# Kernel optimization log

Hardware: AMD Instinct MI355X
Metric: run time of the kernel (lower is better)

## Reference

```python
import jax, jax.numpy as jnp
from jax import lax
import numpy as np

B, T, D, S, P = 2048, 64, 512, 256, 11
H1 = (D + S) // 2  # position head hidden = (d_model + state_dim)//2 = 384


def setup_inputs() -> dict:
    key = jax.random.key(0)
    ks = jax.random.split(key, 8)
    return {
        "price_features": jax.random.normal(ks[0], (B, T, D), jnp.float32),
        "u": jax.random.uniform(ks[1], (B, T, P), jnp.float32),  # gumbel uniform noise
        "W1": 0.02 * jax.random.normal(ks[2], (H1, D + S), jnp.float32),
        "b1": jnp.zeros((H1,), jnp.float32),
        "W2": 0.02 * jax.random.normal(ks[3], (P, H1), jnp.float32),
        "b2": jnp.zeros((P,), jnp.float32),
        "temperature": jnp.float32(1.0),
        "W_ih": 0.05 * jax.random.normal(ks[4], (3 * S, D + 1), jnp.float32),
        "b_ih": jnp.zeros((3 * S,), jnp.float32),
        "W_hh": 0.05 * jax.random.normal(ks[5], (3 * S, S), jnp.float32),
        "b_hh": jnp.zeros((3 * S,), jnp.float32),
        "h0": jax.random.normal(ks[6], (S,), jnp.float32),  # strategy_state_init
    }


def reference(price_features, u, W1, b1, W2, b2, temperature, W_ih, b_ih, W_hh, b_hh, h0):
    pos_vals = jnp.arange(P, dtype=jnp.float32)
    batch = price_features.shape[0]
    h_init = jnp.broadcast_to(h0, (batch, S))

    def step(h, xs):
        feat, u_t = xs  # feat: [B,D], u_t: [B,P]
        combined = jnp.concatenate([feat, h], axis=-1)          # [B, D+S]
        hidden = jax.nn.relu(combined @ W1.T + b1)              # [B, H1]
        logits = hidden @ W2.T + b2                             # [B, P]
        gumbel = -jnp.log(-jnp.log(u_t + 1e-20) + 1e-20)
        probs = jax.nn.softmax((logits + gumbel) / temperature, axis=-1)
        pos = probs @ pos_vals                                  # [B] expected position
        x = jnp.concatenate([feat, pos[:, None]], axis=-1)      # [B, D+1]
        gi = x @ W_ih.T + b_ih                                  # [B, 3S]
        gh = h @ W_hh.T + b_hh                                  # [B, 3S]
        i_r, i_z, i_n = jnp.split(gi, 3, axis=-1)
        h_r, h_z, h_n = jnp.split(gh, 3, axis=-1)
        r = jax.nn.sigmoid(i_r + h_r)
        z = jax.nn.sigmoid(i_z + h_z)
        n = jnp.tanh(i_n + r * h_n)
        h_new = (1.0 - z) * n + z * h                           # PyTorch GRUCell update
        return h_new, (pos, h_new)

    feats_t = jnp.swapaxes(price_features, 0, 1)  # [T,B,D]
    u_tfirst = jnp.swapaxes(u, 0, 1)              # [T,B,P]
    h_final, (positions, states) = lax.scan(step, h_init, (feats_t, u_tfirst))
    all_expected_positions = jnp.swapaxes(positions, 0, 1)  # [B,T]
    all_strategy_states = jnp.swapaxes(states, 0, 1)        # [B,T,S]
    return all_expected_positions, all_strategy_states, h_final
```

## Files before the change

### kernel.cpp

```cpp
#include <hip/hip_runtime.h>
#include <stdint.h>

#define B_  2048
#define T_  64
#define D_  512
#define S_  256
#define P_  11
#define H1_ 384
#define NG_ 1152
#define KH_ 256

typedef unsigned short ushort_t;
typedef __attribute__((ext_vector_type(4))) float    f32x4;
typedef __attribute__((ext_vector_type(8))) __bf16   bf16x8;
typedef __attribute__((ext_vector_type(8))) unsigned short u16x8;

static __device__ __forceinline__ ushort_t f2bf(float f) {
    uint32_t u = __builtin_bit_cast(uint32_t, f);
    u += 0x7fffu + ((u >> 16) & 1u);
    return (ushort_t)(u >> 16);
}
static __device__ __forceinline__ float bf2f(ushort_t h) {
    uint32_t u = ((uint32_t)h) << 16;
    return __builtin_bit_cast(float, u);
}
static __device__ __forceinline__ u16x8 ntload8(const ushort_t* p) {
    return __builtin_nontemporal_load((const u16x8*)p);
}
static __device__ __forceinline__ void gload16(const ushort_t* g, ushort_t* l) {
    __builtin_amdgcn_global_load_lds(
        (const __attribute__((address_space(1))) uint32_t*)(const void*)g,
        (__attribute__((address_space(3))) uint32_t*)(void*)l,
        16, 0, 0);
}


__global__ __launch_bounds__(256) void convert_feat(
        const float* __restrict__ feat,
        ushort_t* __restrict__ featS) {
    int base = blockIdx.x * 1024 + threadIdx.x;
    #pragma unroll
    for (int k = 0; k < 4; ++k) {
        int o = base + k * 256;
        int tile = o >> 10;
        int s = o & 1023;
        int row = s >> 3, slot = s & 7;
        int mtile = tile >> 3, kt = tile & 7;
        int col = kt * 64 + (((slot ^ (row & 7))) << 3);
        const float* gp = feat + (size_t)(mtile * 128 + row) * 512 + col;
        f32x4 f0 = *(const f32x4*)gp;
        f32x4 f1 = *(const f32x4*)(gp + 4);
        u16x8 ov;
        #pragma unroll
        for (int j = 0; j < 4; ++j) { ov[j] = f2bf(f0[j]); ov[4 + j] = f2bf(f1[j]); }
        __builtin_nontemporal_store(ov, (u16x8*)(featS + (size_t)o * 8));
    }
}

__global__ void pack_weights(const float* __restrict__ W1,
                             const float* __restrict__ Wih,
                             const float* __restrict__ Whh,
                             ushort_t* __restrict__ WcatS,
                             ushort_t* __restrict__ WhBp) {
    int idx = blockIdx.x * 256 + threadIdx.x;
    const int tot1 = NG_ * D_;
    if (idx < tot1) {
        int tile = idx >> 13;
        int e = idx & 8191;
        int row = e >> 6, slot = (e >> 3) & 7, j = e & 7;
        int ntile = tile >> 3, kt = tile & 7;
        int col = kt * 64 + ((slot ^ (row & 7)) << 3) + j;
        int n = ntile * 128 + row;
        float v = (n < H1_) ? W1[n * 768 + col] : Wih[(n - H1_) * 513 + col];
        WcatS[idx] = f2bf(v);
    } else {
        int i = idx - tot1;
        int j  = i & 7;
        int l  = (i >> 3) & 63;
        int kc = (i >> 9) & 7;
        int nt = i >> 12;
        int row = nt * 16 + (l & 15);
        int col = kc * 32 + (l >> 4) * 8 + j;
        float v = (row < H1_) ? W1[row * 768 + 512 + col] : Whh[(row - H1_) * 256 + col];
        WhBp[i] = f2bf(v);
    }
}

__global__ __launch_bounds__(256) void gemm_pre(
        const ushort_t* __restrict__ featS,
        const ushort_t* __restrict__ WcatS,
        ushort_t* __restrict__ pre) {
    __shared__ __attribute__((aligned(16))) ushort_t As[8192];
    __shared__ __attribute__((aligned(16))) ushort_t Bs[8192];

    int bx = blockIdx.x;
    int xcd = bx & 7, slt = bx >> 3;
    int mt = (slt / 9) * 8 + xcd;
    int ntb = slt % 9;
    int m0 = mt * 128, n0 = ntb * 128;

    int tid = threadIdx.x;
    int lane = tid & 63, wave = tid >> 6;
    int wr = wave >> 1, wc = wave & 1;
    int l15 = lane & 15, q = lane >> 4;

    const ushort_t* Abase = featS + (size_t)mt * 8 * 8192 + (size_t)(lane << 3);
    const ushort_t* Bbase = WcatS + (size_t)ntb * 8 * 8192 + (size_t)(lane << 3);

    f32x4 acc[4][4];
    #pragma unroll
    for (int i = 0; i < 4; ++i)
        #pragma unroll
        for (int j = 0; j < 4; ++j)
            acc[i][j] = (f32x4){0.f, 0.f, 0.f, 0.f};

    const int swz = (l15 & 7) << 4;

    for (int kt = 0; kt < 8; ++kt) {
        #pragma unroll
        for (int i = 0; i < 4; ++i) {
            int c = wave * 4 + i;
            gload16(Abase + (size_t)kt * 8192 + (c << 9), &As[c << 9]);
            gload16(Bbase + (size_t)kt * 8192 + (c << 9), &Bs[c << 9]);
        }
        __syncthreads();
        #pragma unroll
        for (int kc = 0; kc < 2; ++kc) {
            const int coff = (kc * 64 + q * 16) ^ swz;
            bf16x8 af[4], bfr[4];
            #pragma unroll
            for (int i = 0; i < 4; ++i)
                af[i] = __builtin_bit_cast(bf16x8, *(const u16x8*)(
                    (const char*)As + (wr * 64 + i * 16 + l15) * 128 + coff));
            #pragma unroll
            for (int j = 0; j < 4; ++j)
                bfr[j] = __builtin_bit_cast(bf16x8, *(const u16x8*)(
                    (const char*)Bs + (wc * 64 + j * 16 + l15) * 128 + coff));
            #pragma unroll
            for (int i = 0; i < 4; ++i)
                #pragma unroll
                for (int j = 0; j < 4; ++j)
                    acc[i][j] = __builtin_amdgcn_mfma_f32_16x16x32_bf16(
                        af[i], bfr[j], acc[i][j], 0, 0, 0);
        }
        __syncthreads();
    }
    #pragma unroll
    for (int i = 0; i < 4; ++i) {
        #pragma unroll
        for (int r = 0; r < 4; ++r) {
            int m = m0 + wr * 64 + i * 16 + q * 4 + r;
            int orow = (m & 63) * 2048 + (m >> 6);
            ushort_t* op = pre + (size_t)orow * NG_ + n0 + wc * 64 + l15;
            #pragma unroll
            for (int j = 0; j < 4; ++j)
                __builtin_nontemporal_store(f2bf(acc[i][j][r]), &op[j * 16]);
        }
    }
}

__global__ __launch_bounds__(1024, 4) void recurrent(
        const float* __restrict__ u,
        const float* __restrict__ b1,
        const float* __restrict__ W2,
        const float* __restrict__ b2,
        const float* __restrict__ temp_p,
        const float* __restrict__ Wih,
        const float* __restrict__ bih,
        const float* __restrict__ bhh,
        const float* __restrict__ h0,
        const ushort_t* __restrict__ WhBp,
        const ushort_t* __restrict__ pre,
        float* __restrict__ out_pos,
        float* __restrict__ out_states,
        float* __restrict__ out_hfin) {
    __shared__ __attribute__((aligned(16))) ushort_t gates[8][1160];
    __shared__ __attribute__((aligned(16))) ushort_t preg[8][1160];
    __shared__ __attribute__((aligned(16))) float    hf[8][256];
    __shared__ __attribute__((aligned(16))) ushort_t hb[16][264];
    __shared__ __attribute__((aligned(16))) ushort_t hidb[16][392];
    __shared__ __attribute__((aligned(16))) ushort_t w2s[16][392];
    __shared__ __attribute__((aligned(16))) float    b1s[384];
    __shared__ __attribute__((aligned(16))) float    wps[768];
    __shared__ __attribute__((aligned(16))) float    bihs[768];
    __shared__ __attribute__((aligned(16))) float    bhhs[768];
    __shared__ float    b2s[16];
    __shared__ float    logit_s[8][17];
    __shared__ float    pos_s[8];
    __shared__ float    u_s[8][12];

    const int tid  = threadIdx.x;
    const int lane = tid & 63, wave = tid >> 6;
    const int l15  = lane & 15, q = lane >> 4;
    const int row8 = tid >> 7;
    const int ln128 = tid & 127;
    const int b0 = blockIdx.x * 8;

    for (int i = tid; i < 384; i += 1024) b1s[i] = b1[i];
    for (int i = tid; i < 768; i += 1024) {
        wps[i]  = Wih[i * 513 + 512];
        bihs[i] = bih[i];
        bhhs[i] = bhh[i];
    }
    if (tid < 11) b2s[tid] = b2[tid];
    for (int i = tid; i < 16 * 392; i += 1024) {
        int r = i / 392, c = i - r * 392;
        float v = (r < 11 && c < 384) ? W2[r * 384 + c] : 0.f;
        w2s[r][c] = f2bf(v);
    }
    for (int i = tid; i < 8 * 256; i += 1024) {
        int m = i >> 8, s = i & 255;
        float v = h0[s];
        hf[m][s] = v;
        hb[m][s] = f2bf(v);
    }
    for (int i = tid; i < 8 * 264; i += 1024) {
        int m = 8 + i / 264;
        hb[m][i % 264] = 0;
    }
    for (int i = tid; i < 8 * 392; i += 1024) {
        int m = 8 + i / 392;
        hidb[m][i % 392] = 0;
    }
    float tinv = 1.0f / temp_p[0];

    u16x8 pr[2];
    {
        const size_t prow = (size_t)b0;
        #pragma unroll
        for (int r = 0; r < 2; ++r) {
            int c = tid + (r << 10);
            if (c < 1152) {
                int row = c / 144, off = c - row * 144;
                pr[r] = ntload8(pre + (prow + row) * NG_ + (size_t)off * 8);
            }
        }
    }
    float uval = 0.f;
    const int um = tid / 11, up = tid - um * 11;
    if (tid < 88) uval = u[((size_t)(b0 + um) * 64 + 0) * 11 + up];
    __syncthreads();

    for (int t = 0; t < 64; ++t) {
        #pragma unroll
        for (int r = 0; r < 2; ++r) {
            int c = tid + (r << 10);
            if (c < 1152) {
                int row = c / 144, off = c - row * 144;
                *(u16x8*)&preg[row][off * 8] = pr[r];
            }
        }
        if (tid < 88) u_s[um][up] = uval;

        bf16x8 af[8];
        #pragma unroll
        for (int kc = 0; kc < 8; ++kc)
            af[kc] = __builtin_bit_cast(bf16x8, *(const u16x8*)&hb[l15][kc * 32 + q * 8]);

        for (int nt = wave; nt < 24; nt += 16) {
            f32x4 acc = (f32x4){0.f, 0.f, 0.f, 0.f};
            const ushort_t* wp = WhBp + (((size_t)nt * 8) << 9) + (lane << 3);
            #pragma unroll
            for (int kc = 0; kc < 8; ++kc) {
                bf16x8 bfr = __builtin_bit_cast(bf16x8, *(const u16x8*)(wp + ((size_t)kc << 9)));
                acc = __builtin_amdgcn_mfma_f32_16x16x32_bf16(af[kc], bfr, acc, 0, 0, 0);
            }
            if (q < 2) {
                int n = nt * 16 + l15;
                #pragma unroll
                for (int r = 0; r < 4; ++r)
                    gates[q * 4 + r][n] = f2bf(acc[r]);
            }
        }
        __syncthreads();

        if (ln128 < 48) {
            int c = ln128 << 3;
            u16x8 g8 = *(const u16x8*)&gates[row8][c];
            u16x8 p8 = *(const u16x8*)&preg[row8][c];
            f32x4 ba = *(const f32x4*)&b1s[c];
            f32x4 bb = *(const f32x4*)&b1s[c + 4];
            u16x8 o;
            #pragma unroll
            for (int jj = 0; jj < 8; ++jj) {
                float bv = (jj < 4) ? ba[jj] : bb[jj - 4];
                float v = bf2f(g8[jj]) + bf2f(p8[jj]) + bv;
                o[jj] = f2bf(fmaxf(v, 0.f));
            }
            *(u16x8*)&hidb[row8][c] = o;
        }
        __syncthreads();

        if (wave == 0) {
            f32x4 lacc = (f32x4){0.f, 0.f, 0.f, 0.f};
            #pragma unroll
            for (int kc = 0; kc < 12; ++kc) {
                bf16x8 ha = __builtin_bit_cast(bf16x8,
                    *(const u16x8*)&hidb[l15][kc * 32 + q * 8]);
                bf16x8 wb = __builtin_bit_cast(bf16x8,
                    *(const u16x8*)&w2s[l15][kc * 32 + q * 8]);
                lacc = __builtin_amdgcn_mfma_f32_16x16x32_bf16(ha, wb, lacc, 0, 0, 0);
            }
            if (q < 2) {
                #pragma unroll
                for (int r = 0; r < 4; ++r)
                    logit_s[q * 4 + r][l15] = lacc[r];
            }
            __builtin_amdgcn_s_waitcnt(0);
            if (lane < 8) {
                int m = lane;
                float lg[11];
                float mx = -1e30f;
                #pragma unroll
                for (int p = 0; p < 11; ++p) {
                    float uu = u_s[m][p];
                    float g = -__logf(-__logf(uu + 1e-20f) + 1e-20f);
                    float a = (logit_s[m][p] + b2s[p] + g) * tinv;
                    lg[p] = a;
                    mx = fmaxf(mx, a);
                }
                float se = 0.f, sp = 0.f;
                #pragma unroll
                for (int p = 0; p < 11; ++p) {
                    float e = __expf(lg[p] - mx);
                    se += e;
                    sp += e * (float)p;
                }
                float pos = sp / se;
                pos_s[m] = pos;
                __builtin_nontemporal_store(pos, &out_pos[(size_t)(b0 + m) * 64 + t]);
            }
        } else {
            for (int nt = 23 + wave; nt < 72; nt += 15) {
                f32x4 acc = (f32x4){0.f, 0.f, 0.f, 0.f};
                const ushort_t* wp = WhBp + (((size_t)nt * 8) << 9) + (lane << 3);
                #pragma unroll
                for (int kc = 0; kc < 8; ++kc) {
                    bf16x8 bfr = __builtin_bit_cast(bf16x8, *(const u16x8*)(wp + ((size_t)kc << 9)));
                    acc = __builtin_amdgcn_mfma_f32_16x16x32_bf16(af[kc], bfr, acc, 0, 0, 0);
                }
                if (q < 2) {
                    int n = nt * 16 + l15;
                    #pragma unroll
                    for (int r = 0; r < 4; ++r)
                        gates[q * 4 + r][n] = f2bf(acc[r]);
                }
            }
        }

        if (t < 63) {
            const size_t prow = (size_t)(t + 1) * 2048 + b0;
            #pragma unroll
            for (int r = 0; r < 2; ++r) {
                int c = tid + (r << 10);
                if (c < 1152) {
                    int row = c / 144, off = c - row * 144;
                    pr[r] = ntload8(pre + (prow + row) * NG_ + (size_t)off * 8);
                }
            }
            if (tid < 88) uval = u[((size_t)(b0 + um) * 64 + (t + 1)) * 11 + up];
        }
        __syncthreads();

        {
            float pos = pos_s[row8];
            float* st = out_states + ((size_t)(b0 + row8) * 64 + t) * 256;
            #pragma unroll
            for (int j = 0; j < 2; ++j) {
                int s = ln128 + (j << 7);
                float ar  = bf2f(preg[row8][384 + s]) + bihs[s]
                          + bf2f(gates[row8][384 + s]) + bhhs[s];
                float az  = bf2f(preg[row8][640 + s]) + bihs[256 + s]
                          + bf2f(gates[row8][640 + s]) + bhhs[256 + s];
                float in0 = bf2f(preg[row8][896 + s]) + bihs[512 + s];
                float gn  = bf2f(gates[row8][896 + s]) + bhhs[512 + s];
                float hp  = hf[row8][s];
                float rr = __builtin_amdgcn_rcpf(1.f + __expf(-(ar + pos * wps[s])));
                float zz = __builtin_amdgcn_rcpf(1.f + __expf(-(az + pos * wps[256 + s])));
                float xn = in0 + pos * wps[512 + s] + rr * gn;
                float e2 = __expf(2.f * xn);
                float nn = 1.f - 2.f * __builtin_amdgcn_rcpf(e2 + 1.f);
                float hnew = (1.f - zz) * nn + zz * hp;
                hf[row8][s] = hnew;
                hb[row8][s] = f2bf(hnew);
                __builtin_nontemporal_store(hnew, st + s);
            }
        }
        __syncthreads();
    }

    for (int i = tid; i < 8 * 256; i += 1024) {
        int m = i >> 8, s = i & 255;
        __builtin_nontemporal_store(hf[m][s], &out_hfin[(size_t)(b0 + m) * 256 + s]);
    }
}

extern "C" void kernel_launch(void* const* d_in, const int* in_sizes, int n_in,
                              void* d_out, int out_size, void* d_ws, size_t ws_size,
                              hipStream_t stream) {
    const float* feat = (const float*)d_in[0];
    const float* u    = (const float*)d_in[1];
    const float* W1   = (const float*)d_in[2];
    const float* b1   = (const float*)d_in[3];
    const float* W2   = (const float*)d_in[4];
    const float* b2   = (const float*)d_in[5];
    const float* temp = (const float*)d_in[6];
    const float* Wih  = (const float*)d_in[7];
    const float* bih  = (const float*)d_in[8];
    const float* Whh  = (const float*)d_in[9];
    const float* bhh  = (const float*)d_in[10];
    const float* h0   = (const float*)d_in[11];

    ushort_t* WcatS = (ushort_t*)d_ws;
    ushort_t* WhBp  = WcatS + NG_ * D_;
    ushort_t* pre   = WhBp + NG_ * KH_;
    ushort_t* featS = pre + (size_t)T_ * B_ * NG_;

    float* out_pos    = (float*)d_out;
    float* out_states = out_pos + (size_t)B_ * T_;
    float* out_hfin   = out_states + (size_t)B_ * T_ * S_;

    pack_weights<<<3456, 256, 0, stream>>>(W1, Wih, Whh, WcatS, WhBp);
    convert_feat<<<8192, 256, 0, stream>>>(feat, featS);
    gemm_pre<<<9216, 256, 0, stream>>>(featS, WcatS, pre);
    recurrent<<<256, 1024, 0, stream>>>(u, b1, W2, b2, temp, Wih, bih, bhh, h0,
                                        WhBp, pre, out_pos, out_states, out_hfin);
}
```

Before: 1.107 ms.

## Pre-pack GEMM operands in MFMA fragment order and double-buffer recurrent prefetch

Feature and weight tensors are now packed directly in per-lane MFMA fragment order, so gemm_pre reads its operands straight from global memory into registers and no longer stages them through LDS with barriers. The pre-activation output is written in batch-major order, so each recurrent block reads contiguous rows across timesteps. In the recurrent kernel, the hidden-layer ReLU is fused into the W1 MFMA tile epilogue, which removes a separate gate pass. The next step's pre-activations and noise are double-buffered in shared memory, which eliminates a copy at the top of each step. The cost is that gemm_pre gives up LDS reuse and relies on cache hits, loading each operand fragment separately per wave.

```diff
diff --git a/kernel.cpp b/kernel.cpp
--- a/kernel.cpp
+++ b/kernel.cpp
@@ -27,52 +27,55 @@
 static __device__ __forceinline__ u16x8 ntload8(const ushort_t* p) {
     return __builtin_nontemporal_load((const u16x8*)p);
 }
-static __device__ __forceinline__ void gload16(const ushort_t* g, ushort_t* l) {
-    __builtin_amdgcn_global_load_lds(
-        (const __attribute__((address_space(1))) uint32_t*)(const void*)g,
-        (__attribute__((address_space(3))) uint32_t*)(void*)l,
-        16, 0, 0);
-}
 
 
 __global__ __launch_bounds__(256) void convert_feat(
         const float* __restrict__ feat,
-        ushort_t* __restrict__ featS) {
+        ushort_t* __restrict__ featP) {
     int base = blockIdx.x * 1024 + threadIdx.x;
     #pragma unroll
     for (int k = 0; k < 4; ++k) {
         int o = base + k * 256;
-        int tile = o >> 10;
-        int s = o & 1023;
-        int row = s >> 3, slot = s & 7;
-        int mtile = tile >> 3, kt = tile & 7;
-        int col = kt * 64 + (((slot ^ (row & 7))) << 3);
-        const float* gp = feat + (size_t)(mtile * 128 + row) * 512 + col;
-        f32x4 f0 = *(const f32x4*)gp;
-        f32x4 f1 = *(const f32x4*)(gp + 4);
+        int mt = o >> 13;
+        int f = o & 8191;
+        int ln = f & 63;
+        int i = (f >> 6) & 3;
+        int half = (f >> 8) & 1;
+        int kc = (f >> 9) & 1;
+        int kt = f >> 10;
+        int row = half * 64 + i * 16 + (ln & 15);
+        int col = kt * 64 + kc * 32 + ((ln >> 4) << 3);
+        const float* gp = feat + (size_t)(mt * 128 + row) * 512 + col;
+        f32x4 f0 = __builtin_nontemporal_load((const f32x4*)gp);
+        f32x4 f1 = __builtin_nontemporal_load((const f32x4*)(gp + 4));
         u16x8 ov;
         #pragma unroll
         for (int j = 0; j < 4; ++j) { ov[j] = f2bf(f0[j]); ov[4 + j] = f2bf(f1[j]); }
-        __builtin_nontemporal_store(ov, (u16x8*)(featS + (size_t)o * 8));
+        __builtin_nontemporal_store(ov, (u16x8*)(featP + (size_t)o * 8));
     }
 }
 
 __global__ void pack_weights(const float* __restrict__ W1,
                              const float* __restrict__ Wih,
                              const float* __restrict__ Whh,
-                             ushort_t* __restrict__ WcatS,
+                             ushort_t* __restrict__ WcatP,
                              ushort_t* __restrict__ WhBp) {
     int idx = blockIdx.x * 256 + threadIdx.x;
     const int tot1 = NG_ * D_;
     if (idx < tot1) {
-        int tile = idx >> 13;
-        int e = idx & 8191;
-        int row = e >> 6, slot = (e >> 3) & 7, j = e & 7;
-        int ntile = tile >> 3, kt = tile & 7;
-        int col = kt * 64 + ((slot ^ (row & 7)) << 3) + j;
+        int o = idx >> 3, j = idx & 7;
+        int ntile = o >> 13;
+        int f = o & 8191;
+        int ln = f & 63;
+        int i = (f >> 6) & 3;
+        int half = (f >> 8) & 1;
+        int kc = (f >> 9) & 1;
+        int kt = f >> 10;
+        int row = half * 64 + i * 16 + (ln & 15);
+        int col = kt * 64 + kc * 32 + ((ln >> 4) << 3) + j;
         int n = ntile * 128 + row;
         float v = (n < H1_) ? W1[n * 768 + col] : Wih[(n - H1_) * 513 + col];
-        WcatS[idx] = f2bf(v);
+        WcatP[idx] = f2bf(v);
     } else {
         int i = idx - tot1;
         int j  = i & 7;
@@ -86,13 +89,10 @@
     }
 }
 
-__global__ __launch_bounds__(256) void gemm_pre(
-        const ushort_t* __restrict__ featS,
-        const ushort_t* __restrict__ WcatS,
+__global__ __launch_bounds__(256, 3) void gemm_pre(
+        const ushort_t* __restrict__ featP,
+        const ushort_t* __restrict__ WcatP,
         ushort_t* __restrict__ pre) {
-    __shared__ __attribute__((aligned(16))) ushort_t As[8192];
-    __shared__ __attribute__((aligned(16))) ushort_t Bs[8192];
-
     int bx = blockIdx.x;
     int xcd = bx & 7, slt = bx >> 3;
     int mt = (slt / 9) * 8 + xcd;
@@ -104,8 +104,8 @@
     int wr = wave >> 1, wc = wave & 1;
     int l15 = lane & 15, q = lane >> 4;
 
-    const ushort_t* Abase = featS + (size_t)mt * 8 * 8192 + (size_t)(lane << 3);
-    const ushort_t* Bbase = WcatS + (size_t)ntb * 8 * 8192 + (size_t)(lane << 3);
+    const ushort_t* Ab = featP + ((size_t)mt << 16) + (size_t)(lane << 3);
+    const ushort_t* Bb = WcatP + ((size_t)ntb << 16) + (size_t)(lane << 3);
 
     f32x4 acc[4][4];
     #pragma unroll
@@ -114,28 +114,19 @@
         for (int j = 0; j < 4; ++j)
             acc[i][j] = (f32x4){0.f, 0.f, 0.f, 0.f};
 
-    const int swz = (l15 & 7) << 4;
-
+    #pragma unroll
     for (int kt = 0; kt < 8; ++kt) {
         #pragma unroll
-        for (int i = 0; i < 4; ++i) {
-            int c = wave * 4 + i;
-            gload16(Abase + (size_t)kt * 8192 + (c << 9), &As[c << 9]);
-            gload16(Bbase + (size_t)kt * 8192 + (c << 9), &Bs[c << 9]);
-        }
-        __syncthreads();
-        #pragma unroll
         for (int kc = 0; kc < 2; ++kc) {
-            const int coff = (kc * 64 + q * 16) ^ swz;
             bf16x8 af[4], bfr[4];
             #pragma unroll
             for (int i = 0; i < 4; ++i)
                 af[i] = __builtin_bit_cast(bf16x8, *(const u16x8*)(
-                    (const char*)As + (wr * 64 + i * 16 + l15) * 128 + coff));
+                    Ab + ((((kt * 2 + kc) * 2 + wr) * 4 + i) << 9)));
             #pragma unroll
             for (int j = 0; j < 4; ++j)
                 bfr[j] = __builtin_bit_cast(bf16x8, *(const u16x8*)(
-                    (const char*)Bs + (wc * 64 + j * 16 + l15) * 128 + coff));
+                    Bb + ((((kt * 2 + kc) * 2 + wc) * 4 + j) << 9)));
             #pragma unroll
             for (int i = 0; i < 4; ++i)
                 #pragma unroll
@@ -143,15 +134,13 @@
                     acc[i][j] = __builtin_amdgcn_mfma_f32_16x16x32_bf16(
                         af[i], bfr[j], acc[i][j], 0, 0, 0);
         }
-        __syncthreads();
     }
     #pragma unroll
     for (int i = 0; i < 4; ++i) {
         #pragma unroll
         for (int r = 0; r < 4; ++r) {
             int m = m0 + wr * 64 + i * 16 + q * 4 + r;
-            int orow = (m & 63) * 2048 + (m >> 6);
-            ushort_t* op = pre + (size_t)orow * NG_ + n0 + wc * 64 + l15;
+            ushort_t* op = pre + (size_t)m * NG_ + n0 + wc * 64 + l15;
             #pragma unroll
             for (int j = 0; j < 4; ++j)
                 __builtin_nontemporal_store(f2bf(acc[i][j][r]), &op[j * 16]);
@@ -174,8 +163,8 @@
         float* __restrict__ out_pos,
         float* __restrict__ out_states,
         float* __restrict__ out_hfin) {
-    __shared__ __attribute__((aligned(16))) ushort_t gates[8][1160];
-    __shared__ __attribute__((aligned(16))) ushort_t preg[8][1160];
+    __shared__ __attribute__((aligned(16))) ushort_t gates[8][776];
+    __shared__ __attribute__((aligned(16))) ushort_t preg[2][8][1160];
     __shared__ __attribute__((aligned(16))) float    hf[8][256];
     __shared__ __attribute__((aligned(16))) ushort_t hb[16][264];
     __shared__ __attribute__((aligned(16))) ushort_t hidb[16][392];
@@ -187,7 +176,7 @@
     __shared__ float    b2s[16];
     __shared__ float    logit_s[8][17];
     __shared__ float    pos_s[8];
-    __shared__ float    u_s[8][12];
+    __shared__ float    u_s[2][8][12];
 
     const int tid  = threadIdx.x;
     const int lane = tid & 63, wave = tid >> 6;
@@ -224,70 +213,76 @@
     }
     float tinv = 1.0f / temp_p[0];
 
+    const int um = tid / 11, up = tid - um * 11;
     u16x8 pr[2];
     {
-        const size_t prow = (size_t)b0;
         #pragma unroll
         for (int r = 0; r < 2; ++r) {
             int c = tid + (r << 10);
             if (c < 1152) {
                 int row = c / 144, off = c - row * 144;
-                pr[r] = ntload8(pre + (prow + row) * NG_ + (size_t)off * 8);
-            }
-        }
-    }
-    float uval = 0.f;
-    const int um = tid / 11, up = tid - um * 11;
-    if (tid < 88) uval = u[((size_t)(b0 + um) * 64 + 0) * 11 + up];
-    __syncthreads();
-
-    for (int t = 0; t < 64; ++t) {
+                pr[r] = ntload8(pre + ((size_t)(b0 + row) * 64 + 0) * NG_ + (size_t)off * 8);
+            }
+        }
         #pragma unroll
         for (int r = 0; r < 2; ++r) {
             int c = tid + (r << 10);
             if (c < 1152) {
                 int row = c / 144, off = c - row * 144;
-                *(u16x8*)&preg[row][off * 8] = pr[r];
-            }
-        }
-        if (tid < 88) u_s[um][up] = uval;
+                *(u16x8*)&preg[0][row][off * 8] = pr[r];
+            }
+        }
+        if (tid < 88) u_s[0][um][up] = u[((size_t)(b0 + um) * 64 + 0) * 11 + up];
+    }
+    __syncthreads();
+
+    for (int t = 0; t < 64; ++t) {
+        const int cur = t & 1, nxt = cur ^ 1;
 
         bf16x8 af[8];
         #pragma unroll
         for (int kc = 0; kc < 8; ++kc)
             af[kc] = __builtin_bit_cast(bf16x8, *(const u16x8*)&hb[l15][kc * 32 + q * 8]);
 
-        for (int nt = wave; nt < 24; nt += 16) {
+        auto mfma_tile = [&](int nt) -> f32x4 {
+            const ushort_t* wp = WhBp + ((size_t)nt << 12) + (lane << 3);
             f32x4 acc = (f32x4){0.f, 0.f, 0.f, 0.f};
-            const ushort_t* wp = WhBp + (((size_t)nt * 8) << 9) + (lane << 3);
             #pragma unroll
             for (int kc = 0; kc < 8; ++kc) {
-                bf16x8 bfr = __builtin_bit_cast(bf16x8, *(const u16x8*)(wp + ((size_t)kc << 9)));
+                bf16x8 bfr = __builtin_bit_cast(bf16x8, *(const u16x8*)(wp + (kc << 9)));
                 acc = __builtin_amdgcn_mfma_f32_16x16x32_bf16(af[kc], bfr, acc, 0, 0, 0);
             }
+            return acc;
+        };
+        auto do_relu = [&](int nt) {
+            f32x4 acc = mfma_tile(nt);
             if (q < 2) {
                 int n = nt * 16 + l15;
                 #pragma unroll
+                for (int r = 0; r < 4; ++r) {
+                    int row = q * 4 + r;
+                    float v = acc[r] + bf2f(preg[cur][row][n]) + b1s[n];
+                    hidb[row][n] = f2bf(fmaxf(v, 0.f));
+                }
+            }
+        };
+        auto do_gates = [&](int nt) {
+            f32x4 acc = mfma_tile(nt);
+            if (q < 2) {
+                int n = (nt - 24) * 16 + l15;
+                #pragma unroll
                 for (int r = 0; r < 4; ++r)
                     gates[q * 4 + r][n] = f2bf(acc[r]);
             }
-        }
-        __syncthreads();
-
-        if (ln128 < 48) {
-            int c = ln128 << 3;
-            u16x8 g8 = *(const u16x8*)&gates[row8][c];
-            u16x8 p8 = *(const u16x8*)&preg[row8][c];
-            f32x4 ba = *(const f32x4*)&b1s[c];
-            f32x4 bb = *(const f32x4*)&b1s[c + 4];
-            u16x8 o;
-            #pragma unroll
-            for (int jj = 0; jj < 8; ++jj) {
-                float bv = (jj < 4) ? ba[jj] : bb[jj - 4];
-                float v = bf2f(g8[jj]) + bf2f(p8[jj]) + bv;
-                o[jj] = f2bf(fmaxf(v, 0.f));
-            }
-            *(u16x8*)&hidb[row8][c] = o;
+        };
+
+        if (wave == 0) {
+            do_relu(0); do_relu(1); do_relu(2);
+        } else {
+            int nt = 3 + (wave - 1);
+            do_relu(nt);
+            nt += 15;
+            if (nt < 24) do_relu(nt);
         }
         __syncthreads();
 
@@ -313,7 +308,7 @@
                 float mx = -1e30f;
                 #pragma unroll
                 for (int p = 0; p < 11; ++p) {
-                    float uu = u_s[m][p];
+                    float uu = u_s[cur][m][p];
                     float g = -__logf(-__logf(uu + 1e-20f) + 1e-20f);
                     float a = (logit_s[m][p] + b2s[p] + g) * tinv;
                     lg[p] = a;
@@ -331,31 +326,20 @@
                 __builtin_nontemporal_store(pos, &out_pos[(size_t)(b0 + m) * 64 + t]);
             }
         } else {
-            for (int nt = 23 + wave; nt < 72; nt += 15) {
-                f32x4 acc = (f32x4){0.f, 0.f, 0.f, 0.f};
-                const ushort_t* wp = WhBp + (((size_t)nt * 8) << 9) + (lane << 3);
-                #pragma unroll
-                for (int kc = 0; kc < 8; ++kc) {
-                    bf16x8 bfr = __builtin_bit_cast(bf16x8, *(const u16x8*)(wp + ((size_t)kc << 9)));
-                    acc = __builtin_amdgcn_mfma_f32_16x16x32_bf16(af[kc], bfr, acc, 0, 0, 0);
-                }
-                if (q < 2) {
-                    int n = nt * 16 + l15;
-                    #pragma unroll
-                    for (int r = 0; r < 4; ++r)
-                        gates[q * 4 + r][n] = f2bf(acc[r]);
-                }
-            }
-        }
-
+            int nt = 3 + (wave - 1) + 15;
+            while (nt < 24) nt += 15;
+            for (; nt < 72; nt += 15) do_gates(nt);
+        }
+
+        float uval = 0.f;
         if (t < 63) {
-            const size_t prow = (size_t)(t + 1) * 2048 + b0;
             #pragma unroll
             for (int r = 0; r < 2; ++r) {
                 int c = tid + (r << 10);
                 if (c < 1152) {
                     int row = c / 144, off = c - row * 144;
-                    pr[r] = ntload8(pre + (prow + row) * NG_ + (size_t)off * 8);
+                    pr[r] = ntload8(pre + ((size_t)(b0 + row) * 64 + (t + 1)) * NG_
+                                    + (size_t)off * 8);
                 }
             }
             if (tid < 88) uval = u[((size_t)(b0 + um) * 64 + (t + 1)) * 11 + up];
@@ -368,12 +352,12 @@
             #pragma unroll
             for (int j = 0; j < 2; ++j) {
                 int s = ln128 + (j << 7);
-                float ar  = bf2f(preg[row8][384 + s]) + bihs[s]
-                          + bf2f(gates[row8][384 + s]) + bhhs[s];
-                float az  = bf2f(preg[row8][640 + s]) + bihs[256 + s]
-                          + bf2f(gates[row8][640 + s]) + bhhs[256 + s];
-                float in0 = bf2f(preg[row8][896 + s]) + bihs[512 + s];
-                float gn  = bf2f(gates[row8][896 + s]) + bhhs[512 + s];
+                float ar  = bf2f(preg[cur][row8][384 + s]) + bihs[s]
+                          + bf2f(gates[row8][s]) + bhhs[s];
+                float az  = bf2f(preg[cur][row8][640 + s]) + bihs[256 + s]
+                          + bf2f(gates[row8][256 + s]) + bhhs[256 + s];
+                float in0 = bf2f(preg[cur][row8][896 + s]) + bihs[512 + s];
+                float gn  = bf2f(gates[row8][512 + s]) + bhhs[512 + s];
                 float hp  = hf[row8][s];
                 float rr = __builtin_amdgcn_rcpf(1.f + __expf(-(ar + pos * wps[s])));
                 float zz = __builtin_amdgcn_rcpf(1.f + __expf(-(az + pos * wps[256 + s])));
@@ -384,6 +368,17 @@
                 hf[row8][s] = hnew;
                 hb[row8][s] = f2bf(hnew);
                 __builtin_nontemporal_store(hnew, st + s);
+            }
+            if (t < 63) {
+                #pragma unroll
+                for (int r = 0; r < 2; ++r) {
+                    int c = tid + (r << 10);
+                    if (c < 1152) {
+                        int row = c / 144, off = c - row * 144;
+                        *(u16x8*)&preg[nxt][row][off * 8] = pr[r];
+                    }
+                }
+                if (tid < 88) u_s[nxt][um][up] = uval;
             }
         }
         __syncthreads();
@@ -411,18 +406,18 @@
     const float* bhh  = (const float*)d_in[10];
     const float* h0   = (const float*)d_in[11];
 
-    ushort_t* WcatS = (ushort_t*)d_ws;
-    ushort_t* WhBp  = WcatS + NG_ * D_;
+    ushort_t* WcatP = (ushort_t*)d_ws;
+    ushort_t* WhBp  = WcatP + NG_ * D_;
     ushort_t* pre   = WhBp + NG_ * KH_;
-    ushort_t* featS = pre + (size_t)T_ * B_ * NG_;
+    ushort_t* featP = pre + (size_t)T_ * B_ * NG_;
 
     float* out_pos    = (float*)d_out;
     float* out_states = out_pos + (size_t)B_ * T_;
     float* out_hfin   = out_states + (size_t)B_ * T_ * S_;
 
-    pack_weights<<<3456, 256, 0, stream>>>(W1, Wih, Whh, WcatS, WhBp);
-    convert_feat<<<8192, 256, 0, stream>>>(feat, featS);
-    gemm_pre<<<9216, 256, 0, stream>>>(featS, WcatS, pre);
+    pack_weights<<<3456, 256, 0, stream>>>(W1, Wih, Whh, WcatP, WhBp);
+    convert_feat<<<8192, 256, 0, stream>>>(feat, featP);
+    gemm_pre<<<9216, 256, 0, stream>>>(featP, WcatP, pre);
     recurrent<<<256, 1024, 0, stream>>>(u, b1, W2, b2, temp, Wih, bih, bhh, h0,
                                         WhBp, pre, out_pos, out_states, out_hfin);
 }
```

Measured after the change: 1.314 ms. 18.6% more time.
